# Kernel tuning notes

Measured on AMD Instinct MI355X. Metric: run time of the kernel, lower is better.

## Reference

```python
import jax, jax.numpy as jnp
import numpy as np

B, T, D = 2, 2048, 1024
H = 16
HD = D // H  # 64


def setup_inputs() -> dict:
    key = jax.random.key(0)
    ks = jax.random.split(key, 5)
    s = 0.02
    return {
        "x": jax.random.normal(ks[0], (B, T, D), dtype=jnp.float32),
        "Wqkv": jax.random.normal(ks[1], (D, 3 * D), dtype=jnp.float32) * s,
        "bqkv": jnp.zeros((3 * D,), dtype=jnp.float32),
        "Wproj": jax.random.normal(ks[2], (D, D), dtype=jnp.float32) * s,
        "bproj": jnp.zeros((D,), dtype=jnp.float32),
    }


def _rope(q, k, seq_len, head_dim):
    half = head_dim // 2
    idx = jnp.arange(half, dtype=jnp.float32)
    pos = jnp.arange(seq_len, dtype=jnp.float32)[:, None]  # [T,1]
    rates = jnp.power(10000.0, -2.0 * idx / head_dim)       # [half]
    theta = pos * rates                                      # [T,half]
    cos = jnp.cos(theta)
    sin = jnp.sin(theta)

    def apply(x):  # x: [B,H,T,HD]
        x1 = x[..., :half]
        x2 = x[..., half:half * 2]
        return jnp.concatenate([x1 * cos - x2 * sin, x1 * sin + x2 * cos], axis=-1)

    return apply(q), apply(k)


def reference(x, Wqkv, bqkv, Wproj, bproj):
    b, t, c = x.shape
    qkv = x @ Wqkv + bqkv                       # [B,T,3D]
    q, k, v = jnp.split(qkv, 3, axis=-1)
    q = q.reshape(b, t, H, HD).transpose(0, 2, 1, 3)  # [B,H,T,HD]
    k = k.reshape(b, t, H, HD).transpose(0, 2, 1, 3)
    v = v.reshape(b, t, H, HD).transpose(0, 2, 1, 3)
    q, k = _rope(q, k, t, HD)
    scale = HD ** -0.5
    scores = jnp.einsum('bhqd,bhkd->bhqk', q, k) * scale
    causal = jnp.tril(jnp.ones((t, t), dtype=bool))
    scores = jnp.where(causal, scores, jnp.float32(-jnp.inf))
    attn = jax.nn.softmax(scores, axis=-1)
    y = jnp.einsum('bhqk,bhkd->bhqd', attn, v)  # [B,H,T,HD]
    y = y.transpose(0, 2, 1, 3).reshape(b, t, c)
    return y @ Wproj + bproj
```

## Files before the change

### kernel.cpp

```cpp
#include <hip/hip_runtime.h>
#include <hip/hip_bf16.h>
#include <cstdint>

#define BB 2
#define TT 2048
#define DD 1024
#define HH 16
#define HD 64
#define BT (BB*TT)
#define QKV_N (3*DD)

typedef __attribute__((ext_vector_type(8))) short  short8;
typedef __attribute__((ext_vector_type(4))) float  f32x4;
typedef __attribute__((ext_vector_type(16))) float f32x16;

static __device__ __forceinline__ ushort f2bf(float f) {
    union { float f; uint32_t u; } v; v.f = f;
    uint32_t u = v.u;
    return (ushort)((u + 0x7FFFu + ((u >> 16) & 1u)) >> 16);
}

typedef const __attribute__((address_space(1))) uint32_t* gp1_t;
typedef __attribute__((address_space(3))) uint32_t* lp3_t;
static __device__ __forceinline__ void gload_lds16(const void* g, void* l) {
    __builtin_amdgcn_global_load_lds((gp1_t)g, (lp3_t)l, 16, 0, 0);
}

static __device__ __forceinline__ uint32_t cvtpk_bf16(float a, float b) {
    uint32_t r;
    asm volatile("v_cvt_pk_bf16_f32 %0, %1, %2" : "=v"(r) : "v"(a), "v"(b));
    return r;
}
static __device__ __forceinline__ void pl32swap(uint32_t& a, uint32_t& b) {
    asm volatile("v_permlane32_swap_b32 %0, %1" : "+v"(a), "+v"(b));
}
static __device__ __forceinline__ float fexp2(float x) {
    float r; asm("v_exp_f32 %0, %1" : "=v"(r) : "v"(x)); return r;
}

static __device__ __forceinline__ f32x16 mfma32(short8 a, short8 b, f32x16 c) {
    return __builtin_amdgcn_mfma_f32_32x32x16_bf16(a, b, c, 0, 0, 0);
}

#define QSCALE 0.18033688011112042f

__global__ __launch_bounds__(256) void f32_to_bf16(
    const float* __restrict__ in, ushort* __restrict__ out, int n8)
{
    const int i = blockIdx.x * 256 + threadIdx.x;
    if (i >= n8) return;
    float4 v0 = *(const float4*)(in + (size_t)i * 8);
    float4 v1 = *(const float4*)(in + (size_t)i * 8 + 4);
    ushort o[8] = {f2bf(v0.x), f2bf(v0.y), f2bf(v0.z), f2bf(v0.w),
                   f2bf(v1.x), f2bf(v1.y), f2bf(v1.z), f2bf(v1.w)};
    *(short8*)(out + (size_t)i * 8) = *(const short8*)o;
}

__global__ __launch_bounds__(256) void rope_tab(float2* __restrict__ ctab)
{
    const int idx = blockIdx.x * 256 + threadIdx.x;
    const int i = idx & 31;
    const int t = idx >> 5;
    const float rate = powf(10000.0f, -(float)i * (1.0f / 32.0f));
    const float th = (float)t * rate;
    ctab[idx] = make_float2(cosf(th), sinf(th));
}

__global__ __launch_bounds__(256) void transpose_w_bf16(
    const float* __restrict__ W, ushort* __restrict__ Wt, int K, int N)
{
    __shared__ ushort Ws[64][72];
    const int n0 = blockIdx.x * 64;
    const int k0 = blockIdx.y * 64;
    const int tid = threadIdx.x;

    #pragma unroll
    for (int it = 0; it < 4; ++it) {
        const int r  = it * 16 + (tid >> 4);
        const int c4 = (tid & 15) * 4;
        float4 v = *(const float4*)&W[(size_t)(k0 + r) * N + n0 + c4];
        Ws[c4 + 0][r] = f2bf(v.x);
        Ws[c4 + 1][r] = f2bf(v.y);
        Ws[c4 + 2][r] = f2bf(v.z);
        Ws[c4 + 3][r] = f2bf(v.w);
    }
    __syncthreads();
    #pragma unroll
    for (int it = 0; it < 2; ++it) {
        const int rn = it * 32 + (tid >> 3);
        const int c8 = (tid & 7) * 8;
        *(short8*)&Wt[(size_t)(n0 + rn) * K + k0 + c8] = *(const short8*)&Ws[rn][c8];
    }
}

__global__ __launch_bounds__(256) void gemm_proj(
    const ushort* __restrict__ A, const ushort* __restrict__ Bt,
    const float* __restrict__ bias, float* __restrict__ C,
    int M, int N, int K)
{
    __shared__ __align__(16) ushort As[128 * 64];
    __shared__ __align__(16) ushort Bs[128 * 64];

    const int nbx = N >> 7;
    const int nwg = (M >> 7) * nbx;
    const int cpx = nwg >> 3;
    const int bid = blockIdx.x;
    const int lb  = (bid & 7) * cpx + (bid >> 3);
    const int n0 = (lb % nbx) * 128;
    const int m0 = (lb / nbx) * 128;

    const int tid = threadIdx.x;
    const int w  = tid >> 6, l = tid & 63;
    const int lr = l & 15,  lg = l >> 4;
    const int wm = w >> 1,  wn = w & 1;

    f32x4 acc[4][4] = {};

    for (int k0 = 0; k0 < K; k0 += 64) {
        #pragma unroll
        for (int i = 0; i < 4; ++i) {
            const int f = i * 256 + w * 64 + l;
            const int r = f >> 3, c = f & 7;
            gload_lds16(A + (size_t)(m0 + r) * K + k0 + ((c ^ (r & 7)) << 3),
                        &As[(i * 256 + w * 64) * 8]);
        }
        #pragma unroll
        for (int i = 0; i < 4; ++i) {
            const int f = i * 256 + w * 64 + l;
            const int r = f >> 3, c = f & 7;
            gload_lds16(Bt + (size_t)(n0 + r) * K + k0 + ((c ^ (r & 7)) << 3),
                        &Bs[(i * 256 + w * 64) * 8]);
        }
        __syncthreads();

        #pragma unroll
        for (int kk = 0; kk < 2; ++kk) {
            short8 a[4], b[4];
            #pragma unroll
            for (int mi = 0; mi < 4; ++mi) {
                const int row = wm * 64 + mi * 16 + lr;
                const int c   = kk * 4 + lg;
                a[mi] = *(const short8*)&As[row * 64 + ((c ^ (row & 7)) << 3)];
            }
            #pragma unroll
            for (int ni = 0; ni < 4; ++ni) {
                const int row = wn * 64 + ni * 16 + lr;
                const int c   = kk * 4 + lg;
                b[ni] = *(const short8*)&Bs[row * 64 + ((c ^ (row & 7)) << 3)];
            }
            #pragma unroll
            for (int mi = 0; mi < 4; ++mi)
                #pragma unroll
                for (int ni = 0; ni < 4; ++ni)
                    acc[mi][ni] = __builtin_amdgcn_mfma_f32_16x16x32_bf16(
                        a[mi], b[ni], acc[mi][ni], 0, 0, 0);
        }
        __syncthreads();
    }

    #pragma unroll
    for (int mi = 0; mi < 4; ++mi) {
        #pragma unroll
        for (int ni = 0; ni < 4; ++ni) {
            const int n = n0 + wn * 64 + ni * 16 + lr;
            const float bv = bias[n];
            #pragma unroll
            for (int j = 0; j < 4; ++j) {
                const int m = m0 + wm * 64 + mi * 16 + lg * 4 + j;
                C[(size_t)m * N + n] = acc[mi][ni][j] + bv;
            }
        }
    }
}

__global__ __launch_bounds__(256) void gemm_qkv_fused(
    const ushort* __restrict__ A,
    const ushort* __restrict__ Bt,
    const float*  __restrict__ bias,
    const float2* __restrict__ ctab,
    ushort* __restrict__ Qb, ushort* __restrict__ Kswz, ushort* __restrict__ Vswz)
{
    __shared__ __align__(16) ushort As[128 * 64];
    __shared__ __align__(16) ushort Bs[128 * 64];

    const int nbx = QKV_N >> 7;
    const int cpx = ((BT >> 7) * nbx) >> 3;
    const int bid = blockIdx.x;
    const int lb  = (bid & 7) * cpx + (bid >> 3);
    const int n0 = (lb % nbx) * 128;
    const int m0 = (lb / nbx) * 128;

    const int tid = threadIdx.x;
    const int w  = tid >> 6, l = tid & 63;
    const int lr = l & 15,  lg = l >> 4;
    const int wm = w >> 1,  wn = w & 1;

    f32x4 acc[4][4] = {};

    for (int k0 = 0; k0 < DD; k0 += 64) {
        #pragma unroll
        for (int i = 0; i < 4; ++i) {
            const int f = i * 256 + w * 64 + l;
            const int r = f >> 3, c = f & 7;
            gload_lds16(A + (size_t)(m0 + r) * DD + k0 + ((c ^ (r & 7)) << 3),
                        &As[(i * 256 + w * 64) * 8]);
        }
        #pragma unroll
        for (int i = 0; i < 4; ++i) {
            const int f = i * 256 + w * 64 + l;
            const int r = f >> 3, c = f & 7;
            gload_lds16(Bt + (size_t)(n0 + r) * DD + k0 + ((c ^ (r & 7)) << 3),
                        &Bs[(i * 256 + w * 64) * 8]);
        }
        __syncthreads();

        #pragma unroll
        for (int kk = 0; kk < 2; ++kk) {
            short8 a[4], b[4];
            #pragma unroll
            for (int mi = 0; mi < 4; ++mi) {
                const int row = wm * 64 + mi * 16 + lr;
                const int c   = kk * 4 + lg;
                a[mi] = *(const short8*)&As[row * 64 + ((c ^ (row & 7)) << 3)];
            }
            #pragma unroll
            for (int ni = 0; ni < 4; ++ni) {
                const int row = wn * 64 + ni * 16 + lr;
                const int c   = kk * 4 + lg;
                b[ni] = *(const short8*)&Bs[row * 64 + ((c ^ (row & 7)) << 3)];
            }
            #pragma unroll
            for (int mi = 0; mi < 4; ++mi)
                #pragma unroll
                for (int ni = 0; ni < 4; ++ni)
                    acc[mi][ni] = __builtin_amdgcn_mfma_f32_16x16x32_bf16(
                        a[mi], b[ni], acc[mi][ni], 0, 0, 0);
        }
        __syncthreads();
    }

    const int g64  = n0 + wn * 64;
    const int part = g64 >> 10;
    const int h    = (g64 & 1023) >> 6;

    float bv[4];
    #pragma unroll
    for (int ni = 0; ni < 4; ++ni) bv[ni] = bias[g64 + ni * 16 + lr];

    #pragma unroll
    for (int mi = 0; mi < 4; ++mi) {
        #pragma unroll
        for (int j = 0; j < 4; ++j) {
            const int m  = m0 + wm * 64 + mi * 16 + lg * 4 + j;
            const int bb = m >> 11;
            const int t  = m & (TT - 1);
            const int bh = bb * HH + h;
            const float v0 = acc[mi][0][j] + bv[0];
            const float v1 = acc[mi][1][j] + bv[1];
            const float v2 = acc[mi][2][j] + bv[2];
            const float v3 = acc[mi][3][j] + bv[3];

            if (part == 2) {
                ushort* vb = Vswz + (size_t)bh * (TT * HD) + (t >> 6) * 4096
                           + ((t & 63) >> 4) * 512 + ((t >> 3) & 1) * 256
                           + (t & 7) + lr * 8;
                vb[0]    = f2bf(v0);
                vb[128]  = f2bf(v1);
                vb[2048] = f2bf(v2);
                vb[2176] = f2bf(v3);
            } else {
                const float2 cs0 = ctab[t * 32 + lr];
                const float2 cs1 = ctab[t * 32 + 16 + lr];
                float r0 = v0 * cs0.x - v2 * cs0.y;
                float r2 = v0 * cs0.y + v2 * cs0.x;
                float r1 = v1 * cs1.x - v3 * cs1.y;
                float r3 = v1 * cs1.y + v3 * cs1.x;
                if (part == 0) {
                    r0 *= QSCALE; r1 *= QSCALE; r2 *= QSCALE; r3 *= QSCALE;
                    ushort* qb = Qb + (size_t)bh * (TT * HD) + t * HD + lr;
                    qb[0]  = f2bf(r0);
                    qb[16] = f2bf(r1);
                    qb[32] = f2bf(r2);
                    qb[48] = f2bf(r3);
                } else {
                    ushort* kb = Kswz + (size_t)bh * (TT * HD) + (t >> 6) * 4096
                               + ((t >> 5) & 1) * 2048 + (t & 31) * 8
                               + ((lr >> 3) & 1) * 256 + (lr & 7);
                    kb[0]    = f2bf(r0);
                    kb[512]  = f2bf(r1);
                    kb[1024] = f2bf(r2);
                    kb[1536] = f2bf(r3);
                }
            }
        }
    }
}

__global__ __launch_bounds__(256) void attn_wave32(
    const ushort* __restrict__ Qb, const ushort* __restrict__ Kswz,
    const ushort* __restrict__ Vswz, ushort* __restrict__ y)
{
    const int bid = blockIdx.x;
    const int bh  = bid & 31;
    const int j   = bid >> 5;
    const int b   = bh >> 4;
    const int h   = bh & 15;
    const int tid = threadIdx.x;
    const int w   = tid >> 6;
    const int l   = tid & 63;
    const int lq  = l & 31;
    const int hi  = l >> 5;

    const int qt  = (w < 2) ? (j * 2 + w) : (63 - (j * 2 + (w - 2)));
    const int wq0 = qt * 32;
    const int qg  = wq0 + lq;

    const ushort* Kbh = Kswz + (size_t)bh * TT * HD;
    const ushort* Vbh = Vswz + (size_t)bh * TT * HD;

    short8 qf[4];
    {
        const ushort* qrow = Qb + ((size_t)bh * TT + qg) * HD + hi * 8;
        #pragma unroll
        for (int dc = 0; dc < 4; ++dc)
            qf[dc] = *(const short8*)(qrow + dc * 16);
    }

    f32x16 acc0 = {}, acc1 = {};
    float m = -1e30f, lsum = 0.0f;

    const int nt = (wq0 >> 6) + 1;

    for (int t = 0; t < nt; ++t) {
        const int k0 = t * 64;
        const ushort* kb = Kbh + (size_t)t * 4096 + l * 8;
        const ushort* vb = Vbh + (size_t)t * 4096 + l * 8;

        short8 kf0[4], kf1[4], vf0[4], vf1[4];
        #pragma unroll
        for (int dc = 0; dc < 4; ++dc) {
            kf0[dc] = *(const short8*)(kb + dc * 512);
            kf1[dc] = *(const short8*)(kb + (4 + dc) * 512);
            vf0[dc] = *(const short8*)(vb + dc * 512);
            vf1[dc] = *(const short8*)(vb + (4 + dc) * 512);
        }

        f32x16 st0 = {}, st1 = {};
        __builtin_amdgcn_s_setprio(1);
        #pragma unroll
        for (int dc = 0; dc < 4; ++dc) {
            st0 = mfma32(kf0[dc], qf[dc], st0);
            st1 = mfma32(kf1[dc], qf[dc], st1);
        }
        __builtin_amdgcn_s_setprio(0);

        if (t == nt - 1) {
            #pragma unroll
            for (int r = 0; r < 16; ++r) {
                const int kk = k0 + (r & 3) + 8 * (r >> 2) + 4 * hi;
                if (kk > qg)      st0[r] = -1e30f;
                if (kk + 32 > qg) st1[r] = -1e30f;
            }
        }

        float pm;
        {
            float m16[16];
            #pragma unroll
            for (int i = 0; i < 16; ++i) m16[i] = fmaxf(st0[i], st1[i]);
            float m8[8];
            #pragma unroll
            for (int i = 0; i < 8; ++i) m8[i] = fmaxf(m16[i], m16[i + 8]);
            const float a = fmaxf(fmaxf(m8[0], m8[4]), fmaxf(m8[1], m8[5]));
            const float c = fmaxf(fmaxf(m8[2], m8[6]), fmaxf(m8[3], m8[7]));
            pm = fmaxf(a, c);
        }
        pm = fmaxf(pm, __shfl_xor(pm, 32));

        if (!__all(pm - m <= 8.0f)) {
            const float nm    = fmaxf(m, pm);
            const float alpha = fexp2(m - nm);
            m = nm;
            lsum *= alpha;
            #pragma unroll
            for (int r = 0; r < 16; ++r) {
                const float ar = __shfl(alpha, (r & 3) + 8 * (r >> 2) + 4 * hi);
                acc0[r] *= ar; acc1[r] *= ar;
            }
        }

        #pragma unroll
        for (int r = 0; r < 16; ++r) {
            st0[r] = fexp2(st0[r] - m);
            st1[r] = fexp2(st1[r] - m);
        }
        float rs;
        {
            float s16[16];
            #pragma unroll
            for (int i = 0; i < 16; ++i) s16[i] = st0[i] + st1[i];
            float s8[8];
            #pragma unroll
            for (int i = 0; i < 8; ++i) s8[i] = s16[i] + s16[i + 8];
            rs = ((s8[0] + s8[4]) + (s8[1] + s8[5]))
               + ((s8[2] + s8[6]) + (s8[3] + s8[7]));
        }
        rs += __shfl_xor(rs, 32);
        lsum += rs;

        short8 pfr[4];
        #pragma unroll
        for (int sub = 0; sub < 2; ++sub) {
            const f32x16& ps = sub ? st1 : st0;
            uint32_t A0 = cvtpk_bf16(ps[0],  ps[1]);
            uint32_t A1 = cvtpk_bf16(ps[2],  ps[3]);
            uint32_t B0 = cvtpk_bf16(ps[4],  ps[5]);
            uint32_t B1 = cvtpk_bf16(ps[6],  ps[7]);
            uint32_t C0 = cvtpk_bf16(ps[8],  ps[9]);
            uint32_t C1 = cvtpk_bf16(ps[10], ps[11]);
            uint32_t D0 = cvtpk_bf16(ps[12], ps[13]);
            uint32_t D1 = cvtpk_bf16(ps[14], ps[15]);
            pl32swap(A0, B0); pl32swap(A1, B1);
            pl32swap(C0, D0); pl32swap(C1, D1);
            union { uint32_t u[4]; short8 s; } f0, f1;
            f0.u[0] = A0; f0.u[1] = A1; f0.u[2] = B0; f0.u[3] = B1;
            f1.u[0] = C0; f1.u[1] = C1; f1.u[2] = D0; f1.u[3] = D1;
            pfr[sub * 2]     = f0.s;
            pfr[sub * 2 + 1] = f1.s;
        }

        __builtin_amdgcn_s_setprio(1);
        #pragma unroll
        for (int kc = 0; kc < 4; ++kc) {
            acc0 = mfma32(pfr[kc], vf0[kc], acc0);
            acc1 = mfma32(pfr[kc], vf1[kc], acc1);
        }
        __builtin_amdgcn_s_setprio(0);
    }

    const float inv = 1.0f / lsum;
    #pragma unroll
    for (int r = 0; r < 16; ++r) {
        const int row = (r & 3) + 8 * (r >> 2) + 4 * hi;
        const float ir = __shfl(inv, row);
        ushort* yo = y + ((size_t)b * TT + wq0 + row) * DD + h * HD;
        yo[lq]      = f2bf(acc0[r] * ir);
        yo[32 + lq] = f2bf(acc1[r] * ir);
    }
}

extern "C" void kernel_launch(void* const* d_in, const int* in_sizes, int n_in,
                              void* d_out, int out_size, void* d_ws, size_t ws_size,
                              hipStream_t stream)
{
    const float* x     = (const float*)d_in[0];
    const float* Wqkv  = (const float*)d_in[1];
    const float* bqkv  = (const float*)d_in[2];
    const float* Wproj = (const float*)d_in[3];
    const float* bproj = (const float*)d_in[4];
    float* out = (float*)d_out;

    ushort* yb     = (ushort*)d_ws;
    ushort* Qb     = yb     + (size_t)BT * DD;
    ushort* Kswz   = Qb     + (size_t)BB * HH * TT * HD;
    ushort* Vswz   = Kswz   + (size_t)BB * HH * TT * HD;
    ushort* xb     = Vswz   + (size_t)BB * HH * TT * HD;
    ushort* Wqkvt  = xb     + (size_t)BT * DD;
    ushort* Wprojt = Wqkvt  + (size_t)QKV_N * DD;
    float2* ctab   = (float2*)(Wprojt + (size_t)DD * DD);

    f32_to_bf16<<<(BT * DD / 8 + 255) / 256, 256, 0, stream>>>(x, xb, BT * DD / 8);
    rope_tab<<<TT * 32 / 256, 256, 0, stream>>>(ctab);
    {
        dim3 g1(QKV_N / 64, DD / 64);
        transpose_w_bf16<<<g1, 256, 0, stream>>>(Wqkv, Wqkvt, DD, QKV_N);
        dim3 g2(DD / 64, DD / 64);
        transpose_w_bf16<<<g2, 256, 0, stream>>>(Wproj, Wprojt, DD, DD);
    }
    {
        gemm_qkv_fused<<<(BT / 128) * (QKV_N / 128), 256, 0, stream>>>(
            xb, Wqkvt, bqkv, ctab, Qb, Kswz, Vswz);
    }
    {
        attn_wave32<<<512, 256, 0, stream>>>(Qb, Kswz, Vswz, yb);
    }
    {
        gemm_proj<<<(BT / 128) * (DD / 128), 256, 0, stream>>>(
            yb, Wprojt, bproj, out, BT, DD, DD);
    }
}
```

Measured before the change: 123.8 us.

## Split attention KV loop across four waves with LDS softmax merge

The attention kernel now gives each block a single 32-row query tile, with the four waves each handling every fourth KV tile. Partial accumulators, running max and row sums go to shared memory and are merged with a log-sum-exp rescale before writing bf16 output. The grid grows from 512 to 2048 blocks and the longest tiles are scheduled first, aiming to cut the serial per-wave KV loop and even out causal load imbalance. In exchange it adds about 33KB of LDS per block, a block barrier and a merge pass, and the Q tile is loaded by all four waves.

```diff
diff --git a/kernel.cpp b/kernel.cpp
--- a/kernel.cpp
+++ b/kernel.cpp
@@ -296,13 +296,16 @@
     }
 }
 
-__global__ __launch_bounds__(256) void attn_wave32(
+__global__ __launch_bounds__(256) void attn_splitk(
     const ushort* __restrict__ Qb, const ushort* __restrict__ Kswz,
     const ushort* __restrict__ Vswz, ushort* __restrict__ y)
 {
+    __shared__ float Lacc[4][32][64];
+    __shared__ float Lm[4][32], Ll[4][32];
+
     const int bid = blockIdx.x;
     const int bh  = bid & 31;
-    const int j   = bid >> 5;
+    const int qt  = 63 - (bid >> 5);
     const int b   = bh >> 4;
     const int h   = bh & 15;
     const int tid = threadIdx.x;
@@ -311,7 +314,6 @@
     const int lq  = l & 31;
     const int hi  = l >> 5;
 
-    const int qt  = (w < 2) ? (j * 2 + w) : (63 - (j * 2 + (w - 2)));
     const int wq0 = qt * 32;
     const int qg  = wq0 + lq;
 
@@ -331,7 +333,7 @@
 
     const int nt = (wq0 >> 6) + 1;
 
-    for (int t = 0; t < nt; ++t) {
+    for (int t = w; t < nt; t += 4) {
         const int k0 = t * 64;
         const ushort* kb = Kbh + (size_t)t * 4096 + l * 8;
         const ushort* vb = Vbh + (size_t)t * 4096 + l * 8;
@@ -438,14 +440,40 @@
         __builtin_amdgcn_s_setprio(0);
     }
 
-    const float inv = 1.0f / lsum;
     #pragma unroll
     for (int r = 0; r < 16; ++r) {
-        const int row = (r & 3) + 8 * (r >> 2) + 4 * hi;
-        const float ir = __shfl(inv, row);
-        ushort* yo = y + ((size_t)b * TT + wq0 + row) * DD + h * HD;
-        yo[lq]      = f2bf(acc0[r] * ir);
-        yo[32 + lq] = f2bf(acc1[r] * ir);
+        Lacc[w][r][l]      = acc0[r];
+        Lacc[w][r + 16][l] = acc1[r];
+    }
+    if (hi == 0) { Lm[w][lq] = m; Ll[w][lq] = lsum; }
+    __syncthreads();
+
+    const int r0 = w * 8;
+    float invL[8], alf[8][4];
+    #pragma unroll
+    for (int i = 0; i < 8; ++i) {
+        const int rr  = (r0 + i) & 15;
+        const int row = (rr & 3) + 8 * (rr >> 2) + 4 * hi;
+        const float m0v = Lm[0][row], m1v = Lm[1][row];
+        const float m2v = Lm[2][row], m3v = Lm[3][row];
+        const float M = fmaxf(fmaxf(m0v, m1v), fmaxf(m2v, m3v));
+        const float a0 = fexp2(m0v - M), a1 = fexp2(m1v - M);
+        const float a2 = fexp2(m2v - M), a3 = fexp2(m3v - M);
+        const float L = Ll[0][row] * a0 + Ll[1][row] * a1
+                      + Ll[2][row] * a2 + Ll[3][row] * a3;
+        invL[i] = 1.0f / L;
+        alf[i][0] = a0; alf[i][1] = a1; alf[i][2] = a2; alf[i][3] = a3;
+    }
+    #pragma unroll
+    for (int i = 0; i < 8; ++i) {
+        const int r   = r0 + i;
+        const int rr  = r & 15;
+        const int row = (rr & 3) + 8 * (rr >> 2) + 4 * hi;
+        float o = Lacc[0][r][l] * alf[i][0] + Lacc[1][r][l] * alf[i][1]
+                + Lacc[2][r][l] * alf[i][2] + Lacc[3][r][l] * alf[i][3];
+        o *= invL[i];
+        const int d = (r < 16) ? lq : (32 + lq);
+        y[((size_t)b * TT + wq0 + row) * DD + h * HD + d] = f2bf(o);
     }
 }
 
@@ -482,7 +510,7 @@
             xb, Wqkvt, bqkv, ctab, Qb, Kswz, Vswz);
     }
     {
-        attn_wave32<<<512, 256, 0, stream>>>(Qb, Kswz, Vswz, yb);
+        attn_splitk<<<2048, 256, 0, stream>>>(Qb, Kswz, Vswz, yb);
     }
     {
         gemm_proj<<<(BT / 128) * (DD / 128), 256, 0, stream>>>(
```

New measurement: 119.0 us. 1.04x faster.
